# Performance work log

Measured on AMD Instinct MI355X. Metric: run time of the kernel, lower is better.

The kernel has to match this reference:

```python
import jax, jax.numpy as jnp
import numpy as np
import math

D = 768
H = 12
HD = D // H  # 64
B, N = 16, 1024
EPS = 1e-5


def _rope(x, cos, sin):
    # x: [B,N,H,hd]; cos,sin: [1,N,1,hd]
    x1, x2 = x[..., ::2], x[..., 1::2]
    return jnp.concatenate(
        [x1 * cos[..., ::2] - x2 * sin[..., ::2],
         x1 * sin[..., 1::2] + x2 * cos[..., 1::2]], axis=-1)


def setup_inputs() -> dict:
    key = jax.random.key(0)
    ks = jax.random.split(key, 8)
    s = 1.0 / math.sqrt(D)  # xavier-ish scale
    return {
        "x": jax.random.normal(ks[0], (B, N, D), jnp.float32),
        "rope_emb": jax.random.normal(ks[1], (N, HD), jnp.float32),
        "ln_w": jnp.ones((D,), jnp.float32),
        "ln_b": jnp.zeros((D,), jnp.float32),
        "enc_w": jax.random.normal(ks[2], (D, D), jnp.float32) * s,
        "enc_b": jnp.zeros((D,), jnp.float32),
        "qk_w": jax.random.normal(ks[3], (D, D), jnp.float32) * s,
        "qk_b": jnp.zeros((D,), jnp.float32),
        "v_w": jax.random.normal(ks[4], (D, D), jnp.float32) * s,
        "v_b": jnp.zeros((D,), jnp.float32),
        "out_w": jax.random.normal(ks[5], (D, D), jnp.float32) * s,
        "out_b": jnp.zeros((D,), jnp.float32),
        "gate_w": jax.random.normal(ks[6], (D, D), jnp.float32) * s,
        "gate_b": jnp.zeros((D,), jnp.float32),
    }


def reference(x, rope_emb, ln_w, ln_b, enc_w, enc_b, qk_w, qk_b,
              v_w, v_b, out_w, out_b, gate_w, gate_b):
    b, n, d = x.shape
    # Pre-LayerNorm
    mu = jnp.mean(x, axis=-1, keepdims=True)
    var = jnp.mean(jnp.square(x - mu), axis=-1, keepdims=True)
    x_norm = (x - mu) / jnp.sqrt(var + EPS) * ln_w + ln_b
    # sparse latent encoder
    x_latent = jax.nn.relu(x_norm @ enc_w.T + enc_b)
    qk = (x_latent @ qk_w.T + qk_b).reshape(b, n, H, HD)
    v = (x_latent @ v_w.T + v_b).reshape(b, n, H, HD)
    ang = rope_emb[:, :HD]
    cos = jnp.cos(ang)[None, :, None, :]
    sin = jnp.sin(ang)[None, :, None, :]
    qk = _rope(qk, cos, sin)
    # raw (softmax-free) attention, Q=K
    scores = jnp.einsum('bnhd,bmhd->bhnm', qk, qk) / math.sqrt(HD)
    attn = jnp.einsum('bhnm,bmhd->bnhd', scores, v).reshape(b, n, d)
    attn = attn @ out_w.T + out_b
    gate = jax.nn.sigmoid(x_norm @ gate_w.T + gate_b)
    return x + gate * attn
```

## Files before the change

### kernel.cpp

```cpp
#include <hip/hip_runtime.h>

typedef __bf16 bf16;
typedef __bf16 bf16x4 __attribute__((ext_vector_type(4)));
typedef __bf16 bf16x8 __attribute__((ext_vector_type(8)));
typedef float floatx4 __attribute__((ext_vector_type(4)));

#define DD 768
#define NH 12
#define HDIM 64
#define BB 16
#define NN 1024
#define MTOT (BB*NN)
#define WELEM (DD*DD)

__device__ __forceinline__ void async_cp16(const void* g, void* l) {
  __builtin_amdgcn_global_load_lds((const __attribute__((address_space(1))) void*)g,
                                   (__attribute__((address_space(3))) void*)l, 16, 0, 0);
}

__global__ __launch_bounds__(256) void ln_kernel(const float* __restrict__ x,
    const float* __restrict__ w, const float* __restrict__ b, bf16* __restrict__ A) {
  int row = blockIdx.x * 4 + (threadIdx.x >> 6);
  int lane = threadIdx.x & 63;
  const float4* xr = (const float4*)(x + (size_t)row * DD);
  float4 v[3];
  float s = 0.f;
#pragma unroll
  for (int i = 0; i < 3; i++) {
    v[i] = xr[lane + 64 * i];
    s += v[i].x + v[i].y + v[i].z + v[i].w;
  }
#pragma unroll
  for (int o = 32; o; o >>= 1) s += __shfl_xor(s, o);
  float mu = s * (1.f / 768.f);
  float vs = 0.f;
#pragma unroll
  for (int i = 0; i < 3; i++) {
    float dx;
    dx = v[i].x - mu; vs += dx * dx;
    dx = v[i].y - mu; vs += dx * dx;
    dx = v[i].z - mu; vs += dx * dx;
    dx = v[i].w - mu; vs += dx * dx;
  }
#pragma unroll
  for (int o = 32; o; o >>= 1) vs += __shfl_xor(vs, o);
  float rstd = rsqrtf(vs * (1.f / 768.f) + 1e-5f);
  const float4* wv = (const float4*)w;
  const float4* bv = (const float4*)b;
  bf16* Ar = A + (size_t)row * DD;
#pragma unroll
  for (int i = 0; i < 3; i++) {
    int c4 = lane + 64 * i;
    float4 ww = wv[c4], bb = bv[c4];
    bf16x4 pk;
    pk[0] = (bf16)((v[i].x - mu) * rstd * ww.x + bb.x);
    pk[1] = (bf16)((v[i].y - mu) * rstd * ww.y + bb.y);
    pk[2] = (bf16)((v[i].z - mu) * rstd * ww.z + bb.z);
    pk[3] = (bf16)((v[i].w - mu) * rstd * ww.w + bb.w);
    *(bf16x4*)(Ar + c4 * 4) = pk;
  }
}

__global__ __launch_bounds__(256) void convw_kernel(const float* __restrict__ w0,
    const float* __restrict__ w1, const float* __restrict__ w2,
    const float* __restrict__ w3, const float* __restrict__ w4, bf16* __restrict__ out) {
  int i = blockIdx.x * 256 + threadIdx.x;
  int which = i / (WELEM / 4);
  int off = (i % (WELEM / 4)) * 4;
  const float* s = which == 0 ? w0 : which == 1 ? w1 : which == 2 ? w2 : which == 3 ? w3 : w4;
  float4 v = *(const float4*)(s + off);
  bf16x4 pk;
  pk[0] = (bf16)v.x; pk[1] = (bf16)v.y; pk[2] = (bf16)v.z; pk[3] = (bf16)v.w;
  *(bf16x4*)(out + (size_t)i * 4) = pk;
}

template<int EPI>
__device__ __forceinline__ void gemm_body(
    int bm, int bn, int bnl,
    const bf16* __restrict__ Aop, const bf16* __restrict__ W,
    const float* __restrict__ bias,
    bf16* __restrict__ Cb, float* __restrict__ Cf,
    const float* __restrict__ Xres, const bf16* __restrict__ Gate,
    bf16* As, bf16* Bs) {
  int tid = threadIdx.x;
  int wave = tid >> 6, lane = tid & 63;
  int quad = lane >> 4, l16 = lane & 15;
  int wm = wave & 1, wn = wave >> 1;
  int srow = lane >> 2, scol = (lane & 3) * 8;

  const bf16* Ag = Aop + (size_t)(bm * 128 + srow) * DD + scol;
  const bf16* Bg = W + (size_t)(bn * 128 + srow) * DD + scol;

  floatx4 acc[4][4];
#pragma unroll
  for (int i = 0; i < 4; i++)
#pragma unroll
    for (int j = 0; j < 4; j++)
      acc[i][j] = (floatx4){0.f, 0.f, 0.f, 0.f};

  for (int k0 = 0; k0 < DD; k0 += 32) {
    __syncthreads();
#pragma unroll
    for (int it = 0; it < 2; it++) {
      int r0 = (it * 4 + wave) * 16;
      async_cp16(Ag + (size_t)r0 * DD + k0, &As[r0 * 32]);
      async_cp16(Bg + (size_t)r0 * DD + k0, &Bs[r0 * 32]);
    }
    __syncthreads();
    bf16x8 a[4], b[4];
#pragma unroll
    for (int i = 0; i < 4; i++) a[i] = *(const bf16x8*)&As[(wm * 64 + i * 16 + l16) * 32 + quad * 8];
#pragma unroll
    for (int i = 0; i < 4; i++) b[i] = *(const bf16x8*)&Bs[(wn * 64 + i * 16 + l16) * 32 + quad * 8];
    if (EPI == 2) {
#pragma unroll
      for (int mi = 0; mi < 4; mi++)
#pragma unroll
        for (int ni = 0; ni < 4; ni++)
          acc[mi][ni] = __builtin_amdgcn_mfma_f32_16x16x32_bf16(a[mi], b[ni], acc[mi][ni], 0, 0, 0);
    } else {
#pragma unroll
      for (int mi = 0; mi < 4; mi++)
#pragma unroll
        for (int ni = 0; ni < 4; ni++)
          acc[mi][ni] = __builtin_amdgcn_mfma_f32_16x16x32_bf16(b[ni], a[mi], acc[mi][ni], 0, 0, 0);
    }
  }

  if (EPI == 2) {
#pragma unroll
    for (int ni = 0; ni < 4; ni++) {
      int gc = bnl * 128 + wn * 64 + ni * 16 + l16;
      float bz = bias[gc];
      int h = gc >> 6, dd2 = gc & 63;
#pragma unroll
      for (int mi = 0; mi < 4; mi++) {
        int gm0 = bm * 128 + wm * 64 + mi * 16 + quad * 4;
        int b_ = gm0 >> 10, n0 = gm0 & 1023;
        bf16x4 pk;
#pragma unroll
        for (int r = 0; r < 4; r++) pk[r] = (bf16)(acc[mi][ni][r] + bz);
        *(bf16x4*)&Cb[(((size_t)b_ * NH + h) * HDIM + dd2) * NN + n0] = pk;
      }
    }
  } else {
#pragma unroll
    for (int mi = 0; mi < 4; mi++) {
      int gm = bm * 128 + wm * 64 + mi * 16 + l16;
#pragma unroll
      for (int ni = 0; ni < 4; ni++) {
        int gc = bnl * 128 + wn * 64 + ni * 16 + quad * 4;
        float4 bz = *(const float4*)&bias[gc];
        float v0 = acc[mi][ni][0] + bz.x;
        float v1 = acc[mi][ni][1] + bz.y;
        float v2 = acc[mi][ni][2] + bz.z;
        float v3 = acc[mi][ni][3] + bz.w;
        size_t idx = (size_t)gm * DD + gc;
        if (EPI == 4) {
          bf16x4 g = *(const bf16x4*)&Gate[idx];
          float4 xr = *(const float4*)&Xres[idx];
          float4 o;
          o.x = xr.x + (float)g[0] * v0;
          o.y = xr.y + (float)g[1] * v1;
          o.z = xr.z + (float)g[2] * v2;
          o.w = xr.w + (float)g[3] * v3;
          *(float4*)&Cf[idx] = o;
        } else {
          bf16x4 pk;
          if (EPI == 0) {
            pk[0] = (bf16)fmaxf(v0, 0.f); pk[1] = (bf16)fmaxf(v1, 0.f);
            pk[2] = (bf16)fmaxf(v2, 0.f); pk[3] = (bf16)fmaxf(v3, 0.f);
          } else if (EPI == 1) {
            pk[0] = (bf16)v0; pk[1] = (bf16)v1; pk[2] = (bf16)v2; pk[3] = (bf16)v3;
          } else {
            pk[0] = (bf16)(1.f / (1.f + __expf(-v0)));
            pk[1] = (bf16)(1.f / (1.f + __expf(-v1)));
            pk[2] = (bf16)(1.f / (1.f + __expf(-v2)));
            pk[3] = (bf16)(1.f / (1.f + __expf(-v3)));
          }
          *(bf16x4*)&Cb[idx] = pk;
        }
      }
    }
  }
}

template<int EPI_LO, int EPI_HI, int NBN>
__global__ __launch_bounds__(256) void gemm_kernel(
    const bf16* __restrict__ Aop, const bf16* __restrict__ W,
    const float* __restrict__ bias_lo, const float* __restrict__ bias_hi,
    bf16* __restrict__ C_lo, bf16* __restrict__ C_hi, float* __restrict__ Cf,
    const float* __restrict__ Xres, const bf16* __restrict__ Gate) {
  __shared__ bf16 As[128 * 32];
  __shared__ bf16 Bs[128 * 32];
  int blk = blockIdx.x;
  int xcd = blk & 7, slot = blk >> 3;
  int bm = xcd * 16 + slot / NBN;
  int bn = slot % NBN;
  if (NBN == 12 && bn >= 6) {
    gemm_body<EPI_HI>(bm, bn, bn - 6, Aop, W, bias_hi, C_hi, Cf, Xres, Gate, As, Bs);
  } else {
    gemm_body<EPI_LO>(bm, bn, bn, Aop, W, bias_lo, C_lo, Cf, Xres, Gate, As, Bs);
  }
}

__global__ __launch_bounds__(256) void rope_kernel(const bf16* __restrict__ QKraw,
    const float* __restrict__ rope, bf16* __restrict__ QKr, bf16* __restrict__ QKrT) {
  int blk = blockIdx.x;
  int bh = blk >> 7;
  int nc = blk & 127;
  int b_ = bh / NH, h_ = bh % NH;
  int t = threadIdx.x;
  int noff = t >> 5;
  int d = t & 31;
  int n = nc * 8 + noff;
  size_t ibase = ((size_t)(b_ * NN + n)) * DD + h_ * HDIM;
  float x1 = (float)QKraw[ibase + 2 * d];
  float x2 = (float)QKraw[ibase + 2 * d + 1];
  float a0 = rope[n * HDIM + 2 * d];
  float a1 = rope[n * HDIM + 2 * d + 1];
  float o1 = x1 * __cosf(a0) - x2 * __sinf(a0);
  float o2 = x1 * __sinf(a1) + x2 * __cosf(a1);
  size_t obase = ((size_t)(b_ * NN + n)) * DD + h_ * HDIM;
  QKr[obase + d] = (bf16)o1;
  QKr[obase + 32 + d] = (bf16)o2;
  size_t tbase = ((size_t)bh * HDIM + d) * NN + n;
  QKrT[tbase] = (bf16)o1;
  QKrT[tbase + (size_t)32 * NN] = (bf16)o2;
}

__global__ __launch_bounds__(256) void attn_kernel(const bf16* __restrict__ QKr,
    const bf16* __restrict__ QKrT, const bf16* __restrict__ VT, bf16* __restrict__ attn) {
  __shared__ float Tp[64][64];
  __shared__ bf16 Tbf[64][72];
  int bh = blockIdx.x;
  int tid = threadIdx.x, wave = tid >> 6, lane = tid & 63;
  int quad = lane >> 4, l16 = lane & 15;
  const bf16* Qt = QKrT + (size_t)bh * (HDIM * NN);
  const bf16* Vt = VT + (size_t)bh * (HDIM * NN);

  floatx4 acc[4][4];
#pragma unroll
  for (int i = 0; i < 4; i++)
#pragma unroll
    for (int j = 0; j < 4; j++)
      acc[i][j] = (floatx4){0.f, 0.f, 0.f, 0.f};

  int kbase = wave * 256;
#pragma unroll
  for (int k0 = 0; k0 < 256; k0 += 32) {
    bf16x8 a[4], b[4];
#pragma unroll
    for (int i = 0; i < 4; i++) a[i] = *(const bf16x8*)&Qt[(size_t)(i * 16 + l16) * NN + kbase + k0 + quad * 8];
#pragma unroll
    for (int i = 0; i < 4; i++) b[i] = *(const bf16x8*)&Vt[(size_t)(i * 16 + l16) * NN + kbase + k0 + quad * 8];
#pragma unroll
    for (int mi = 0; mi < 4; mi++)
#pragma unroll
      for (int ni = 0; ni < 4; ni++)
        acc[mi][ni] = __builtin_amdgcn_mfma_f32_16x16x32_bf16(a[mi], b[ni], acc[mi][ni], 0, 0, 0);
  }
#pragma unroll
  for (int w = 0; w < 4; w++) {
    if (wave == w) {
#pragma unroll
      for (int mi = 0; mi < 4; mi++)
#pragma unroll
        for (int ni = 0; ni < 4; ni++)
#pragma unroll
          for (int r = 0; r < 4; r++) {
            float val = acc[mi][ni][r];
            float* p = &Tp[mi * 16 + quad * 4 + r][ni * 16 + l16];
            if (w == 0) *p = val; else *p += val;
          }
    }
    __syncthreads();
  }
  for (int e = tid; e < 4096; e += 256) {
    int d1 = e >> 6, d2 = e & 63;
    Tbf[d2][d1] = (bf16)(Tp[d1][d2] * 0.125f);
  }
  __syncthreads();

  int b_ = bh / NH, h_ = bh % NH;
  const bf16* Q = QKr + (size_t)(b_ * NN) * DD + h_ * HDIM;
  bf16* Ao = attn + (size_t)(b_ * NN) * DD + h_ * HDIM;
  bf16x8 Bf[4][2];
#pragma unroll
  for (int ni = 0; ni < 4; ni++)
#pragma unroll
    for (int ks = 0; ks < 2; ks++)
      Bf[ni][ks] = *(const bf16x8*)&Tbf[ni * 16 + l16][ks * 32 + quad * 8];

  for (int mi = 0; mi < 16; mi++) {
    int nrow = wave * 256 + mi * 16;
    bf16x8 a0 = *(const bf16x8*)&Q[(size_t)(nrow + l16) * DD + quad * 8];
    bf16x8 a1 = *(const bf16x8*)&Q[(size_t)(nrow + l16) * DD + 32 + quad * 8];
    floatx4 o[4];
#pragma unroll
    for (int ni = 0; ni < 4; ni++) o[ni] = (floatx4){0.f, 0.f, 0.f, 0.f};
#pragma unroll
    for (int ni = 0; ni < 4; ni++) {
      o[ni] = __builtin_amdgcn_mfma_f32_16x16x32_bf16(a0, Bf[ni][0], o[ni], 0, 0, 0);
      o[ni] = __builtin_amdgcn_mfma_f32_16x16x32_bf16(a1, Bf[ni][1], o[ni], 0, 0, 0);
    }
#pragma unroll
    for (int ni = 0; ni < 4; ni++)
#pragma unroll
      for (int r = 0; r < 4; r++)
        Ao[(size_t)(nrow + quad * 4 + r) * DD + ni * 16 + l16] = (bf16)o[ni][r];
  }
}

extern "C" void kernel_launch(void* const* d_in, const int* in_sizes, int n_in,
                              void* d_out, int out_size, void* d_ws, size_t ws_size,
                              hipStream_t stream) {
  const float* x      = (const float*)d_in[0];
  const float* rope   = (const float*)d_in[1];
  const float* ln_w   = (const float*)d_in[2];
  const float* ln_b   = (const float*)d_in[3];
  const float* enc_w  = (const float*)d_in[4];
  const float* enc_b  = (const float*)d_in[5];
  const float* qk_w   = (const float*)d_in[6];
  const float* qk_b   = (const float*)d_in[7];
  const float* v_w    = (const float*)d_in[8];
  const float* v_b    = (const float*)d_in[9];
  const float* out_w  = (const float*)d_in[10];
  const float* out_b  = (const float*)d_in[11];
  const float* gate_w = (const float*)d_in[12];
  const float* gate_b = (const float*)d_in[13];

  char* w = (char*)d_ws;
  const size_t S = (size_t)MTOT * DD * 2;
  bf16* s0 = (bf16*)(w);
  bf16* s1 = (bf16*)(w + S);
  bf16* s2 = (bf16*)(w + 2 * S);
  bf16* s3 = (bf16*)(w + 3 * S);
  bf16* s4 = (bf16*)(w + 4 * S);
  bf16* s5 = (bf16*)(w + 5 * S);
  bf16* Wb = (bf16*)(w + 6 * S);

  bf16* A = s0;
  bf16* L = s1;
  bf16* Gate = s2;
  bf16* QKraw = s0;
  bf16* QKr = s3;
  bf16* QKrT = s4;
  bf16* VT = s5;
  bf16* attnb = s1;

  ln_kernel<<<dim3(MTOT / 4), dim3(256), 0, stream>>>(x, ln_w, ln_b, A);
  convw_kernel<<<dim3(5 * WELEM / 4 / 256), dim3(256), 0, stream>>>(enc_w, gate_w, qk_w, v_w, out_w, Wb);

  gemm_kernel<0, 3, 12><<<dim3(1536), dim3(256), 0, stream>>>(
      A, Wb, enc_b, gate_b, L, Gate, nullptr, nullptr, nullptr);
  gemm_kernel<1, 2, 12><<<dim3(1536), dim3(256), 0, stream>>>(
      L, Wb + 2 * (size_t)WELEM, qk_b, v_b, QKraw, VT, nullptr, nullptr, nullptr);
  rope_kernel<<<dim3(BB * NH * 128), dim3(256), 0, stream>>>(QKraw, rope, QKr, QKrT);
  attn_kernel<<<dim3(BB * NH), dim3(256), 0, stream>>>(QKr, QKrT, VT, attnb);
  gemm_kernel<4, 4, 6><<<dim3(768), dim3(256), 0, stream>>>(
      attnb, Wb + 4 * (size_t)WELEM, out_b, nullptr, nullptr, nullptr, (float*)d_out, x, Gate);
}
```

Measured before the change: 360.0 us.

## Widen GEMM K-tile with swizzled LDS, vectorize rope transpose, split attention blocks

The GEMM main loop now stages 64-wide K tiles with an XOR-swizzled LDS layout, which halves the barrier count and avoids bank conflicts on fragment reads. The rope kernel processes 128 rows per block with vectorized loads and sincos, and writes the transposed copy through LDS so the global stores are coalesced. The attention kernel launches four blocks per head with XCD-aware mapping, spreading the output phase across more CUs, but each block recomputes the 64x64 K^T V product. LDS use per GEMM block doubles, which may lower occupancy.

```diff
diff --git a/kernel.cpp b/kernel.cpp
--- a/kernel.cpp
+++ b/kernel.cpp
@@ -86,10 +86,11 @@
   int wave = tid >> 6, lane = tid & 63;
   int quad = lane >> 4, l16 = lane & 15;
   int wm = wave & 1, wn = wave >> 1;
-  int srow = lane >> 2, scol = (lane & 3) * 8;
-
-  const bf16* Ag = Aop + (size_t)(bm * 128 + srow) * DD + scol;
-  const bf16* Bg = W + (size_t)(bn * 128 + srow) * DD + scol;
+  int sr = lane >> 3;
+  int smcg = (lane & 7) ^ sr;
+
+  const bf16* Ag = Aop + (size_t)(bm * 128) * DD;
+  const bf16* Bg = W + (size_t)(bn * 128) * DD;
 
   floatx4 acc[4][4];
 #pragma unroll
@@ -98,32 +99,39 @@
     for (int j = 0; j < 4; j++)
       acc[i][j] = (floatx4){0.f, 0.f, 0.f, 0.f};
 
-  for (int k0 = 0; k0 < DD; k0 += 32) {
+  int swzA = (l16 & 7);
+
+  for (int k0 = 0; k0 < DD; k0 += 64) {
     __syncthreads();
 #pragma unroll
-    for (int it = 0; it < 2; it++) {
-      int r0 = (it * 4 + wave) * 16;
-      async_cp16(Ag + (size_t)r0 * DD + k0, &As[r0 * 32]);
-      async_cp16(Bg + (size_t)r0 * DD + k0, &Bs[r0 * 32]);
+    for (int it = 0; it < 4; it++) {
+      int c = it * 4 + wave;
+      int row = c * 8 + sr;
+      async_cp16(Ag + (size_t)row * DD + k0 + smcg * 8, &As[c * 512]);
+      async_cp16(Bg + (size_t)row * DD + k0 + smcg * 8, &Bs[c * 512]);
     }
     __syncthreads();
-    bf16x8 a[4], b[4];
-#pragma unroll
-    for (int i = 0; i < 4; i++) a[i] = *(const bf16x8*)&As[(wm * 64 + i * 16 + l16) * 32 + quad * 8];
-#pragma unroll
-    for (int i = 0; i < 4; i++) b[i] = *(const bf16x8*)&Bs[(wn * 64 + i * 16 + l16) * 32 + quad * 8];
-    if (EPI == 2) {
-#pragma unroll
-      for (int mi = 0; mi < 4; mi++)
-#pragma unroll
-        for (int ni = 0; ni < 4; ni++)
-          acc[mi][ni] = __builtin_amdgcn_mfma_f32_16x16x32_bf16(a[mi], b[ni], acc[mi][ni], 0, 0, 0);
-    } else {
-#pragma unroll
-      for (int mi = 0; mi < 4; mi++)
-#pragma unroll
-        for (int ni = 0; ni < 4; ni++)
-          acc[mi][ni] = __builtin_amdgcn_mfma_f32_16x16x32_bf16(b[ni], a[mi], acc[mi][ni], 0, 0, 0);
+#pragma unroll
+    for (int ks = 0; ks < 2; ks++) {
+      int cg = (ks * 4 + quad) ^ swzA;
+      bf16x8 a[4], b[4];
+#pragma unroll
+      for (int i = 0; i < 4; i++) a[i] = *(const bf16x8*)&As[(wm * 64 + i * 16 + l16) * 64 + cg * 8];
+#pragma unroll
+      for (int i = 0; i < 4; i++) b[i] = *(const bf16x8*)&Bs[(wn * 64 + i * 16 + l16) * 64 + cg * 8];
+      if (EPI == 2) {
+#pragma unroll
+        for (int mi = 0; mi < 4; mi++)
+#pragma unroll
+          for (int ni = 0; ni < 4; ni++)
+            acc[mi][ni] = __builtin_amdgcn_mfma_f32_16x16x32_bf16(a[mi], b[ni], acc[mi][ni], 0, 0, 0);
+      } else {
+#pragma unroll
+        for (int mi = 0; mi < 4; mi++)
+#pragma unroll
+          for (int ni = 0; ni < 4; ni++)
+            acc[mi][ni] = __builtin_amdgcn_mfma_f32_16x16x32_bf16(b[ni], a[mi], acc[mi][ni], 0, 0, 0);
+      }
     }
   }
 
@@ -191,8 +199,8 @@
     const float* __restrict__ bias_lo, const float* __restrict__ bias_hi,
     bf16* __restrict__ C_lo, bf16* __restrict__ C_hi, float* __restrict__ Cf,
     const float* __restrict__ Xres, const bf16* __restrict__ Gate) {
-  __shared__ bf16 As[128 * 32];
-  __shared__ bf16 Bs[128 * 32];
+  __shared__ bf16 As[128 * 64];
+  __shared__ bf16 Bs[128 * 64];
   int blk = blockIdx.x;
   int xcd = blk & 7, slot = blk >> 3;
   int bm = xcd * 16 + slot / NBN;
@@ -204,36 +212,73 @@
   }
 }
 
+#define TLS_S 132
 __global__ __launch_bounds__(256) void rope_kernel(const bf16* __restrict__ QKraw,
     const float* __restrict__ rope, bf16* __restrict__ QKr, bf16* __restrict__ QKrT) {
+  __shared__ bf16 Tls[64 * TLS_S];
   int blk = blockIdx.x;
-  int bh = blk >> 7;
-  int nc = blk & 127;
+  int bh = blk >> 3, nc = blk & 7;
   int b_ = bh / NH, h_ = bh % NH;
+  int nbase = nc * 128;
   int t = threadIdx.x;
-  int noff = t >> 5;
-  int d = t & 31;
-  int n = nc * 8 + noff;
-  size_t ibase = ((size_t)(b_ * NN + n)) * DD + h_ * HDIM;
-  float x1 = (float)QKraw[ibase + 2 * d];
-  float x2 = (float)QKraw[ibase + 2 * d + 1];
-  float a0 = rope[n * HDIM + 2 * d];
-  float a1 = rope[n * HDIM + 2 * d + 1];
-  float o1 = x1 * __cosf(a0) - x2 * __sinf(a0);
-  float o2 = x1 * __sinf(a1) + x2 * __cosf(a1);
-  size_t obase = ((size_t)(b_ * NN + n)) * DD + h_ * HDIM;
-  QKr[obase + d] = (bf16)o1;
-  QKr[obase + 32 + d] = (bf16)o2;
-  size_t tbase = ((size_t)bh * HDIM + d) * NN + n;
-  QKrT[tbase] = (bf16)o1;
-  QKrT[tbase + (size_t)32 * NN] = (bf16)o2;
+  {
+    int n_loc = t >> 1, ch = t & 1;
+    int n = nbase + n_loc;
+    const bf16* src = QKraw + ((size_t)(b_ * NN + n)) * DD + h_ * HDIM + ch * 32;
+    const float* rp = rope + n * HDIM + ch * 32;
+    __attribute__((aligned(16))) bf16 o1[16];
+    __attribute__((aligned(16))) bf16 o2[16];
+#pragma unroll
+    for (int i0 = 0; i0 < 4; i0++) {
+      bf16x8 v = *(const bf16x8*)(src + i0 * 8);
+      float4 r0 = *(const float4*)(rp + i0 * 8);
+      float4 r1 = *(const float4*)(rp + i0 * 8 + 4);
+      float a0s[4] = {r0.x, r0.z, r1.x, r1.z};
+      float a1s[4] = {r0.y, r0.w, r1.y, r1.w};
+#pragma unroll
+      for (int p = 0; p < 4; p++) {
+        float x1 = (float)v[2 * p], x2 = (float)v[2 * p + 1];
+        float s0, c0, s1, c1;
+        __sincosf(a0s[p], &s0, &c0);
+        __sincosf(a1s[p], &s1, &c1);
+        int d = i0 * 4 + p;
+        o1[d] = (bf16)(x1 * c0 - x2 * s0);
+        o2[d] = (bf16)(x1 * s1 + x2 * c1);
+      }
+    }
+    bf16* dst = QKr + ((size_t)(b_ * NN + n)) * DD + h_ * HDIM;
+    *(bf16x8*)&dst[ch * 16]      = *(bf16x8*)&o1[0];
+    *(bf16x8*)&dst[ch * 16 + 8]  = *(bf16x8*)&o1[8];
+    *(bf16x8*)&dst[32 + ch * 16]     = *(bf16x8*)&o2[0];
+    *(bf16x8*)&dst[32 + ch * 16 + 8] = *(bf16x8*)&o2[8];
+#pragma unroll
+    for (int d = 0; d < 16; d++) {
+      Tls[(ch * 16 + d) * TLS_S + n_loc] = o1[d];
+      Tls[(32 + ch * 16 + d) * TLS_S + n_loc] = o2[d];
+    }
+  }
+  __syncthreads();
+  {
+    int c = t >> 2, qn = t & 3;
+    __attribute__((aligned(16))) bf16 buf[32];
+#pragma unroll
+    for (int j = 0; j < 8; j++)
+      *(bf16x4*)&buf[j * 4] = *(const bf16x4*)&Tls[c * TLS_S + qn * 32 + j * 4];
+    bf16* dst = QKrT + ((size_t)bh * HDIM + c) * NN + nbase + qn * 32;
+#pragma unroll
+    for (int j = 0; j < 4; j++)
+      *(bf16x8*)&dst[j * 8] = *(bf16x8*)&buf[j * 8];
+  }
 }
 
 __global__ __launch_bounds__(256) void attn_kernel(const bf16* __restrict__ QKr,
     const bf16* __restrict__ QKrT, const bf16* __restrict__ VT, bf16* __restrict__ attn) {
   __shared__ float Tp[64][64];
   __shared__ bf16 Tbf[64][72];
-  int bh = blockIdx.x;
+  int blk = blockIdx.x;
+  int xcd = blk & 7, s = blk >> 3;
+  int bhl = s >> 2, q = s & 3;
+  int bh = xcd * 24 + bhl;
   int tid = threadIdx.x, wave = tid >> 6, lane = tid & 63;
   int quad = lane >> 4, l16 = lane & 15;
   const bf16* Qt = QKrT + (size_t)bh * (HDIM * NN);
@@ -292,8 +337,9 @@
     for (int ks = 0; ks < 2; ks++)
       Bf[ni][ks] = *(const bf16x8*)&Tbf[ni * 16 + l16][ks * 32 + quad * 8];
 
-  for (int mi = 0; mi < 16; mi++) {
-    int nrow = wave * 256 + mi * 16;
+#pragma unroll
+  for (int mi = 0; mi < 4; mi++) {
+    int nrow = q * 256 + wave * 64 + mi * 16;
     bf16x8 a0 = *(const bf16x8*)&Q[(size_t)(nrow + l16) * DD + quad * 8];
     bf16x8 a1 = *(const bf16x8*)&Q[(size_t)(nrow + l16) * DD + 32 + quad * 8];
     floatx4 o[4];
@@ -356,8 +402,8 @@
       A, Wb, enc_b, gate_b, L, Gate, nullptr, nullptr, nullptr);
   gemm_kernel<1, 2, 12><<<dim3(1536), dim3(256), 0, stream>>>(
       L, Wb + 2 * (size_t)WELEM, qk_b, v_b, QKraw, VT, nullptr, nullptr, nullptr);
-  rope_kernel<<<dim3(BB * NH * 128), dim3(256), 0, stream>>>(QKraw, rope, QKr, QKrT);
-  attn_kernel<<<dim3(BB * NH), dim3(256), 0, stream>>>(QKr, QKrT, VT, attnb);
+  rope_kernel<<<dim3(BB * NH * 8), dim3(256), 0, stream>>>(QKraw, rope, QKr, QKrT);
+  attn_kernel<<<dim3(BB * NH * 4), dim3(256), 0, stream>>>(QKr, QKrT, VT, attnb);
   gemm_kernel<4, 4, 6><<<dim3(768), dim3(256), 0, stream>>>(
       attnb, Wb + 4 * (size_t)WELEM, out_b, nullptr, nullptr, nullptr, (float*)d_out, x, Gate);
 }
```

Result: faster. 339.8 us (-5.6%).

## Fuse prep kernels and RoPE epilogue, double-buffer GEMM, split attention across blocks

Applied to the files above, without the earlier changes.

Merges layernorm and weight conversion into one launch, and folds RoPE into the QK GEMM epilogue, which removes the separate rope kernel and the transposed QK/V buffers. The GEMM gains double-buffered LDS staging with an XOR swizzle and a launch-bounds occupancy hint. Attention now transposes Q and V through LDS inside the kernel and splits each head across 4 blocks (768 instead of 192), so more CUs are busy. The cost is that each of the 4 blocks recomputes the 64x64 K^T V product redundantly, and LDS use is higher.

```diff
diff --git a/kernel.cpp b/kernel.cpp
--- a/kernel.cpp
+++ b/kernel.cpp
@@ -1,6 +1,7 @@
 #include <hip/hip_runtime.h>
 
 typedef __bf16 bf16;
+typedef __bf16 bf16x2 __attribute__((ext_vector_type(2)));
 typedef __bf16 bf16x4 __attribute__((ext_vector_type(4)));
 typedef __bf16 bf16x8 __attribute__((ext_vector_type(8)));
 typedef float floatx4 __attribute__((ext_vector_type(4)));
@@ -18,67 +19,69 @@
                                    (__attribute__((address_space(3))) void*)l, 16, 0, 0);
 }
 
-__global__ __launch_bounds__(256) void ln_kernel(const float* __restrict__ x,
-    const float* __restrict__ w, const float* __restrict__ b, bf16* __restrict__ A) {
-  int row = blockIdx.x * 4 + (threadIdx.x >> 6);
-  int lane = threadIdx.x & 63;
-  const float4* xr = (const float4*)(x + (size_t)row * DD);
-  float4 v[3];
-  float s = 0.f;
-#pragma unroll
-  for (int i = 0; i < 3; i++) {
-    v[i] = xr[lane + 64 * i];
-    s += v[i].x + v[i].y + v[i].z + v[i].w;
-  }
-#pragma unroll
-  for (int o = 32; o; o >>= 1) s += __shfl_xor(s, o);
-  float mu = s * (1.f / 768.f);
-  float vs = 0.f;
-#pragma unroll
-  for (int i = 0; i < 3; i++) {
-    float dx;
-    dx = v[i].x - mu; vs += dx * dx;
-    dx = v[i].y - mu; vs += dx * dx;
-    dx = v[i].z - mu; vs += dx * dx;
-    dx = v[i].w - mu; vs += dx * dx;
-  }
-#pragma unroll
-  for (int o = 32; o; o >>= 1) vs += __shfl_xor(vs, o);
-  float rstd = rsqrtf(vs * (1.f / 768.f) + 1e-5f);
-  const float4* wv = (const float4*)w;
-  const float4* bv = (const float4*)b;
-  bf16* Ar = A + (size_t)row * DD;
-#pragma unroll
-  for (int i = 0; i < 3; i++) {
-    int c4 = lane + 64 * i;
-    float4 ww = wv[c4], bb = bv[c4];
+__global__ __launch_bounds__(256) void prep_kernel(const float* __restrict__ x,
+    const float* __restrict__ lnw, const float* __restrict__ lnb, bf16* __restrict__ A,
+    const float* __restrict__ w0, const float* __restrict__ w1, const float* __restrict__ w2,
+    const float* __restrict__ w3, const float* __restrict__ w4, bf16* __restrict__ Wb) {
+  int blk = blockIdx.x;
+  if (blk < 4096) {
+    int row = blk * 4 + (threadIdx.x >> 6);
+    int lane = threadIdx.x & 63;
+    const float4* xr = (const float4*)(x + (size_t)row * DD);
+    float4 v[3];
+    float s = 0.f;
+#pragma unroll
+    for (int i = 0; i < 3; i++) {
+      v[i] = xr[lane + 64 * i];
+      s += v[i].x + v[i].y + v[i].z + v[i].w;
+    }
+#pragma unroll
+    for (int o = 32; o; o >>= 1) s += __shfl_xor(s, o);
+    float mu = s * (1.f / 768.f);
+    float vs = 0.f;
+#pragma unroll
+    for (int i = 0; i < 3; i++) {
+      float dx;
+      dx = v[i].x - mu; vs += dx * dx;
+      dx = v[i].y - mu; vs += dx * dx;
+      dx = v[i].z - mu; vs += dx * dx;
+      dx = v[i].w - mu; vs += dx * dx;
+    }
+#pragma unroll
+    for (int o = 32; o; o >>= 1) vs += __shfl_xor(vs, o);
+    float rstd = rsqrtf(vs * (1.f / 768.f) + 1e-5f);
+    const float4* wv = (const float4*)lnw;
+    const float4* bv = (const float4*)lnb;
+    bf16* Ar = A + (size_t)row * DD;
+#pragma unroll
+    for (int i = 0; i < 3; i++) {
+      int c4 = lane + 64 * i;
+      float4 ww = wv[c4], bb = bv[c4];
+      bf16x4 pk;
+      pk[0] = (bf16)((v[i].x - mu) * rstd * ww.x + bb.x);
+      pk[1] = (bf16)((v[i].y - mu) * rstd * ww.y + bb.y);
+      pk[2] = (bf16)((v[i].z - mu) * rstd * ww.z + bb.z);
+      pk[3] = (bf16)((v[i].w - mu) * rstd * ww.w + bb.w);
+      *(bf16x4*)(Ar + c4 * 4) = pk;
+    }
+  } else {
+    int i = (blk - 4096) * 256 + threadIdx.x;
+    int which = i / (WELEM / 4);
+    int off = (i % (WELEM / 4)) * 4;
+    const float* s = which == 0 ? w0 : which == 1 ? w1 : which == 2 ? w2 : which == 3 ? w3 : w4;
+    float4 v = *(const float4*)(s + off);
     bf16x4 pk;
-    pk[0] = (bf16)((v[i].x - mu) * rstd * ww.x + bb.x);
-    pk[1] = (bf16)((v[i].y - mu) * rstd * ww.y + bb.y);
-    pk[2] = (bf16)((v[i].z - mu) * rstd * ww.z + bb.z);
-    pk[3] = (bf16)((v[i].w - mu) * rstd * ww.w + bb.w);
-    *(bf16x4*)(Ar + c4 * 4) = pk;
-  }
-}
-
-__global__ __launch_bounds__(256) void convw_kernel(const float* __restrict__ w0,
-    const float* __restrict__ w1, const float* __restrict__ w2,
-    const float* __restrict__ w3, const float* __restrict__ w4, bf16* __restrict__ out) {
-  int i = blockIdx.x * 256 + threadIdx.x;
-  int which = i / (WELEM / 4);
-  int off = (i % (WELEM / 4)) * 4;
-  const float* s = which == 0 ? w0 : which == 1 ? w1 : which == 2 ? w2 : which == 3 ? w3 : w4;
-  float4 v = *(const float4*)(s + off);
-  bf16x4 pk;
-  pk[0] = (bf16)v.x; pk[1] = (bf16)v.y; pk[2] = (bf16)v.z; pk[3] = (bf16)v.w;
-  *(bf16x4*)(out + (size_t)i * 4) = pk;
-}
-
+    pk[0] = (bf16)v.x; pk[1] = (bf16)v.y; pk[2] = (bf16)v.z; pk[3] = (bf16)v.w;
+    *(bf16x4*)(Wb + (size_t)i * 4) = pk;
+  }
+}
+
+#define STG32 4096
 template<int EPI>
 __device__ __forceinline__ void gemm_body(
     int bm, int bn, int bnl,
     const bf16* __restrict__ Aop, const bf16* __restrict__ W,
-    const float* __restrict__ bias,
+    const float* __restrict__ bias, const float* __restrict__ rope,
     bf16* __restrict__ Cb, float* __restrict__ Cf,
     const float* __restrict__ Xres, const bf16* __restrict__ Gate,
     bf16* As, bf16* Bs) {
@@ -86,10 +89,11 @@
   int wave = tid >> 6, lane = tid & 63;
   int quad = lane >> 4, l16 = lane & 15;
   int wm = wave & 1, wn = wave >> 1;
-  int srow = lane >> 2, scol = (lane & 3) * 8;
-
-  const bf16* Ag = Aop + (size_t)(bm * 128 + srow) * DD + scol;
-  const bf16* Bg = W + (size_t)(bn * 128 + srow) * DD + scol;
+  int srow = lane >> 2;
+  int scg = (lane & 3) ^ ((lane >> 3) & 3);
+
+  const bf16* Ag = Aop + ((size_t)(bm * 128) + srow) * DD + scg * 8;
+  const bf16* Bg = W + ((size_t)(bn * 128) + srow) * DD + scg * 8;
 
   floatx4 acc[4][4];
 #pragma unroll
@@ -98,204 +102,197 @@
     for (int j = 0; j < 4; j++)
       acc[i][j] = (floatx4){0.f, 0.f, 0.f, 0.f};
 
-  for (int k0 = 0; k0 < DD; k0 += 32) {
+  int swz = (l16 >> 1) & 3;
+
+#pragma unroll
+  for (int it = 0; it < 2; it++) {
+    int c = it * 4 + wave;
+    async_cp16(Ag + (size_t)(c * 16) * DD, &As[c * 512]);
+    async_cp16(Bg + (size_t)(c * 16) * DD, &Bs[c * 512]);
+  }
+
+  for (int i = 0; i < 24; i++) {
     __syncthreads();
-#pragma unroll
-    for (int it = 0; it < 2; it++) {
-      int r0 = (it * 4 + wave) * 16;
-      async_cp16(Ag + (size_t)r0 * DD + k0, &As[r0 * 32]);
-      async_cp16(Bg + (size_t)r0 * DD + k0, &Bs[r0 * 32]);
-    }
-    __syncthreads();
+    if (i < 23) {
+      int k0 = (i + 1) * 32;
+      int so = ((i + 1) & 1) * STG32;
+#pragma unroll
+      for (int it = 0; it < 2; it++) {
+        int c = it * 4 + wave;
+        async_cp16(Ag + (size_t)(c * 16) * DD + k0, &As[so + c * 512]);
+        async_cp16(Bg + (size_t)(c * 16) * DD + k0, &Bs[so + c * 512]);
+      }
+    }
+    int bo = (i & 1) * STG32;
+    int cg = quad ^ swz;
     bf16x8 a[4], b[4];
 #pragma unroll
-    for (int i = 0; i < 4; i++) a[i] = *(const bf16x8*)&As[(wm * 64 + i * 16 + l16) * 32 + quad * 8];
-#pragma unroll
-    for (int i = 0; i < 4; i++) b[i] = *(const bf16x8*)&Bs[(wn * 64 + i * 16 + l16) * 32 + quad * 8];
-    if (EPI == 2) {
-#pragma unroll
-      for (int mi = 0; mi < 4; mi++)
-#pragma unroll
-        for (int ni = 0; ni < 4; ni++)
-          acc[mi][ni] = __builtin_amdgcn_mfma_f32_16x16x32_bf16(a[mi], b[ni], acc[mi][ni], 0, 0, 0);
-    } else {
-#pragma unroll
-      for (int mi = 0; mi < 4; mi++)
-#pragma unroll
-        for (int ni = 0; ni < 4; ni++)
-          acc[mi][ni] = __builtin_amdgcn_mfma_f32_16x16x32_bf16(b[ni], a[mi], acc[mi][ni], 0, 0, 0);
-    }
-  }
-
-  if (EPI == 2) {
+    for (int j = 0; j < 4; j++) a[j] = *(const bf16x8*)&As[bo + (wm * 64 + j * 16 + l16) * 32 + cg * 8];
+#pragma unroll
+    for (int j = 0; j < 4; j++) b[j] = *(const bf16x8*)&Bs[bo + (wn * 64 + j * 16 + l16) * 32 + cg * 8];
+#pragma unroll
+    for (int mi = 0; mi < 4; mi++)
+#pragma unroll
+      for (int ni = 0; ni < 4; ni++)
+        acc[mi][ni] = __builtin_amdgcn_mfma_f32_16x16x32_bf16(b[ni], a[mi], acc[mi][ni], 0, 0, 0);
+  }
+
+#pragma unroll
+  for (int mi = 0; mi < 4; mi++) {
+    int gm = bm * 128 + wm * 64 + mi * 16 + l16;
 #pragma unroll
     for (int ni = 0; ni < 4; ni++) {
-      int gc = bnl * 128 + wn * 64 + ni * 16 + l16;
-      float bz = bias[gc];
-      int h = gc >> 6, dd2 = gc & 63;
-#pragma unroll
-      for (int mi = 0; mi < 4; mi++) {
-        int gm0 = bm * 128 + wm * 64 + mi * 16 + quad * 4;
-        int b_ = gm0 >> 10, n0 = gm0 & 1023;
+      int gc = bnl * 128 + wn * 64 + ni * 16 + quad * 4;
+      float4 bz = *(const float4*)&bias[gc];
+      float v0 = acc[mi][ni][0] + bz.x;
+      float v1 = acc[mi][ni][1] + bz.y;
+      float v2 = acc[mi][ni][2] + bz.z;
+      float v3 = acc[mi][ni][3] + bz.w;
+      size_t idx = (size_t)gm * DD + gc;
+      if (EPI == 4) {
+        bf16x4 g = *(const bf16x4*)&Gate[idx];
+        float4 xr = *(const float4*)&Xres[idx];
+        float4 o;
+        o.x = xr.x + (float)g[0] * v0;
+        o.y = xr.y + (float)g[1] * v1;
+        o.z = xr.z + (float)g[2] * v2;
+        o.w = xr.w + (float)g[3] * v3;
+        *(float4*)&Cf[idx] = o;
+      } else if (EPI == 5) {
+        int n = gm & (NN - 1);
+        int h = gc >> 6, c0 = gc & 63;
+        int j0 = c0 >> 1;
+        float4 ang = *(const float4*)&rope[n * HDIM + c0];
+        float s0, cc0, s1, cc1, s2, cc2, s3, cc3;
+        __sincosf(ang.x, &s0, &cc0);
+        __sincosf(ang.y, &s1, &cc1);
+        __sincosf(ang.z, &s2, &cc2);
+        __sincosf(ang.w, &s3, &cc3);
+        bf16x2 lo, hi;
+        lo[0] = (bf16)(v0 * cc0 - v1 * s0);
+        lo[1] = (bf16)(v2 * cc2 - v3 * s2);
+        hi[0] = (bf16)(v0 * s1 + v1 * cc1);
+        hi[1] = (bf16)(v2 * s3 + v3 * cc3);
+        bf16* base = Cb + (size_t)gm * DD + h * HDIM;
+        *(bf16x2*)&base[j0] = lo;
+        *(bf16x2*)&base[32 + j0] = hi;
+      } else {
         bf16x4 pk;
-#pragma unroll
-        for (int r = 0; r < 4; r++) pk[r] = (bf16)(acc[mi][ni][r] + bz);
-        *(bf16x4*)&Cb[(((size_t)b_ * NH + h) * HDIM + dd2) * NN + n0] = pk;
+        if (EPI == 0) {
+          pk[0] = (bf16)fmaxf(v0, 0.f); pk[1] = (bf16)fmaxf(v1, 0.f);
+          pk[2] = (bf16)fmaxf(v2, 0.f); pk[3] = (bf16)fmaxf(v3, 0.f);
+        } else if (EPI == 1) {
+          pk[0] = (bf16)v0; pk[1] = (bf16)v1; pk[2] = (bf16)v2; pk[3] = (bf16)v3;
+        } else {
+          pk[0] = (bf16)(1.f / (1.f + __expf(-v0)));
+          pk[1] = (bf16)(1.f / (1.f + __expf(-v1)));
+          pk[2] = (bf16)(1.f / (1.f + __expf(-v2)));
+          pk[3] = (bf16)(1.f / (1.f + __expf(-v3)));
+        }
+        *(bf16x4*)&Cb[idx] = pk;
       }
     }
-  } else {
-#pragma unroll
-    for (int mi = 0; mi < 4; mi++) {
-      int gm = bm * 128 + wm * 64 + mi * 16 + l16;
-#pragma unroll
-      for (int ni = 0; ni < 4; ni++) {
-        int gc = bnl * 128 + wn * 64 + ni * 16 + quad * 4;
-        float4 bz = *(const float4*)&bias[gc];
-        float v0 = acc[mi][ni][0] + bz.x;
-        float v1 = acc[mi][ni][1] + bz.y;
-        float v2 = acc[mi][ni][2] + bz.z;
-        float v3 = acc[mi][ni][3] + bz.w;
-        size_t idx = (size_t)gm * DD + gc;
-        if (EPI == 4) {
-          bf16x4 g = *(const bf16x4*)&Gate[idx];
-          float4 xr = *(const float4*)&Xres[idx];
-          float4 o;
-          o.x = xr.x + (float)g[0] * v0;
-          o.y = xr.y + (float)g[1] * v1;
-          o.z = xr.z + (float)g[2] * v2;
-          o.w = xr.w + (float)g[3] * v3;
-          *(float4*)&Cf[idx] = o;
-        } else {
-          bf16x4 pk;
-          if (EPI == 0) {
-            pk[0] = (bf16)fmaxf(v0, 0.f); pk[1] = (bf16)fmaxf(v1, 0.f);
-            pk[2] = (bf16)fmaxf(v2, 0.f); pk[3] = (bf16)fmaxf(v3, 0.f);
-          } else if (EPI == 1) {
-            pk[0] = (bf16)v0; pk[1] = (bf16)v1; pk[2] = (bf16)v2; pk[3] = (bf16)v3;
-          } else {
-            pk[0] = (bf16)(1.f / (1.f + __expf(-v0)));
-            pk[1] = (bf16)(1.f / (1.f + __expf(-v1)));
-            pk[2] = (bf16)(1.f / (1.f + __expf(-v2)));
-            pk[3] = (bf16)(1.f / (1.f + __expf(-v3)));
-          }
-          *(bf16x4*)&Cb[idx] = pk;
-        }
-      }
-    }
   }
 }
 
 template<int EPI_LO, int EPI_HI, int NBN>
-__global__ __launch_bounds__(256) void gemm_kernel(
+__global__ __launch_bounds__(256, 4) void gemm_kernel(
     const bf16* __restrict__ Aop, const bf16* __restrict__ W,
     const float* __restrict__ bias_lo, const float* __restrict__ bias_hi,
+    const float* __restrict__ rope,
     bf16* __restrict__ C_lo, bf16* __restrict__ C_hi, float* __restrict__ Cf,
     const float* __restrict__ Xres, const bf16* __restrict__ Gate) {
-  __shared__ bf16 As[128 * 32];
-  __shared__ bf16 Bs[128 * 32];
+  __shared__ bf16 As[2 * STG32];
+  __shared__ bf16 Bs[2 * STG32];
   int blk = blockIdx.x;
   int xcd = blk & 7, slot = blk >> 3;
   int bm = xcd * 16 + slot / NBN;
   int bn = slot % NBN;
   if (NBN == 12 && bn >= 6) {
-    gemm_body<EPI_HI>(bm, bn, bn - 6, Aop, W, bias_hi, C_hi, Cf, Xres, Gate, As, Bs);
+    gemm_body<EPI_HI>(bm, bn, bn - 6, Aop, W, bias_hi, rope, C_hi, Cf, Xres, Gate, As, Bs);
   } else {
-    gemm_body<EPI_LO>(bm, bn, bn, Aop, W, bias_lo, C_lo, Cf, Xres, Gate, As, Bs);
-  }
-}
-
-__global__ __launch_bounds__(256) void rope_kernel(const bf16* __restrict__ QKraw,
-    const float* __restrict__ rope, bf16* __restrict__ QKr, bf16* __restrict__ QKrT) {
+    gemm_body<EPI_LO>(bm, bn, bn, Aop, W, bias_lo, rope, C_lo, Cf, Xres, Gate, As, Bs);
+  }
+}
+
+#define TQS 136
+__global__ __launch_bounds__(256, 2) void attn_kernel(const bf16* __restrict__ QKr,
+    const bf16* __restrict__ V, bf16* __restrict__ attn) {
+  __shared__ bf16 Qt[64 * TQS];
+  __shared__ bf16 Vt[64 * TQS];
+  __shared__ bf16 Tbf[64 * 72];
   int blk = blockIdx.x;
-  int bh = blk >> 7;
-  int nc = blk & 127;
+  int xcd = blk & 7, s = blk >> 3;
+  int bhl = s >> 2, q = s & 3;
+  int bh = xcd * 24 + bhl;
   int b_ = bh / NH, h_ = bh % NH;
-  int t = threadIdx.x;
-  int noff = t >> 5;
-  int d = t & 31;
-  int n = nc * 8 + noff;
-  size_t ibase = ((size_t)(b_ * NN + n)) * DD + h_ * HDIM;
-  float x1 = (float)QKraw[ibase + 2 * d];
-  float x2 = (float)QKraw[ibase + 2 * d + 1];
-  float a0 = rope[n * HDIM + 2 * d];
-  float a1 = rope[n * HDIM + 2 * d + 1];
-  float o1 = x1 * __cosf(a0) - x2 * __sinf(a0);
-  float o2 = x1 * __sinf(a1) + x2 * __cosf(a1);
-  size_t obase = ((size_t)(b_ * NN + n)) * DD + h_ * HDIM;
-  QKr[obase + d] = (bf16)o1;
-  QKr[obase + 32 + d] = (bf16)o2;
-  size_t tbase = ((size_t)bh * HDIM + d) * NN + n;
-  QKrT[tbase] = (bf16)o1;
-  QKrT[tbase + (size_t)32 * NN] = (bf16)o2;
-}
-
-__global__ __launch_bounds__(256) void attn_kernel(const bf16* __restrict__ QKr,
-    const bf16* __restrict__ QKrT, const bf16* __restrict__ VT, bf16* __restrict__ attn) {
-  __shared__ float Tp[64][64];
-  __shared__ bf16 Tbf[64][72];
-  int bh = blockIdx.x;
   int tid = threadIdx.x, wave = tid >> 6, lane = tid & 63;
   int quad = lane >> 4, l16 = lane & 15;
-  const bf16* Qt = QKrT + (size_t)bh * (HDIM * NN);
-  const bf16* Vt = VT + (size_t)bh * (HDIM * NN);
-
-  floatx4 acc[4][4];
-#pragma unroll
-  for (int i = 0; i < 4; i++)
-#pragma unroll
-    for (int j = 0; j < 4; j++)
-      acc[i][j] = (floatx4){0.f, 0.f, 0.f, 0.f};
-
-  int kbase = wave * 256;
-#pragma unroll
-  for (int k0 = 0; k0 < 256; k0 += 32) {
-    bf16x8 a[4], b[4];
-#pragma unroll
-    for (int i = 0; i < 4; i++) a[i] = *(const bf16x8*)&Qt[(size_t)(i * 16 + l16) * NN + kbase + k0 + quad * 8];
-#pragma unroll
-    for (int i = 0; i < 4; i++) b[i] = *(const bf16x8*)&Vt[(size_t)(i * 16 + l16) * NN + kbase + k0 + quad * 8];
-#pragma unroll
-    for (int mi = 0; mi < 4; mi++)
-#pragma unroll
-      for (int ni = 0; ni < 4; ni++)
-        acc[mi][ni] = __builtin_amdgcn_mfma_f32_16x16x32_bf16(a[mi], b[ni], acc[mi][ni], 0, 0, 0);
-  }
-#pragma unroll
-  for (int w = 0; w < 4; w++) {
-    if (wave == w) {
-#pragma unroll
-      for (int mi = 0; mi < 4; mi++)
-#pragma unroll
-        for (int ni = 0; ni < 4; ni++)
-#pragma unroll
-          for (int r = 0; r < 4; r++) {
-            float val = acc[mi][ni][r];
-            float* p = &Tp[mi * 16 + quad * 4 + r][ni * 16 + l16];
-            if (w == 0) *p = val; else *p += val;
-          }
-    }
+
+  const bf16* Qbase = QKr + (size_t)(b_ * NN) * DD + h_ * HDIM;
+  const bf16* Vbase = V + (size_t)(b_ * NN) * DD + h_ * HDIM;
+
+  floatx4 acc1[4];
+#pragma unroll
+  for (int i = 0; i < 4; i++) acc1[i] = (floatx4){0.f, 0.f, 0.f, 0.f};
+
+  int p = tid & 63, dq = tid >> 6;
+
+  for (int c = 0; c < 8; c++) {
+    int n0 = c * 128 + p * 2;
+    bf16x8 q0a = *(const bf16x8*)&Qbase[(size_t)n0 * DD + dq * 16];
+    bf16x8 q0b = *(const bf16x8*)&Qbase[(size_t)n0 * DD + dq * 16 + 8];
+    bf16x8 q1a = *(const bf16x8*)&Qbase[(size_t)(n0 + 1) * DD + dq * 16];
+    bf16x8 q1b = *(const bf16x8*)&Qbase[(size_t)(n0 + 1) * DD + dq * 16 + 8];
+    bf16x8 v0a = *(const bf16x8*)&Vbase[(size_t)n0 * DD + dq * 16];
+    bf16x8 v0b = *(const bf16x8*)&Vbase[(size_t)n0 * DD + dq * 16 + 8];
+    bf16x8 v1a = *(const bf16x8*)&Vbase[(size_t)(n0 + 1) * DD + dq * 16];
+    bf16x8 v1b = *(const bf16x8*)&Vbase[(size_t)(n0 + 1) * DD + dq * 16 + 8];
     __syncthreads();
-  }
-  for (int e = tid; e < 4096; e += 256) {
-    int d1 = e >> 6, d2 = e & 63;
-    Tbf[d2][d1] = (bf16)(Tp[d1][d2] * 0.125f);
+    int nl = p * 2;
+#pragma unroll
+    for (int j = 0; j < 8; j++) {
+      bf16x2 qa; qa[0] = q0a[j]; qa[1] = q1a[j];
+      bf16x2 qb; qb[0] = q0b[j]; qb[1] = q1b[j];
+      bf16x2 va; va[0] = v0a[j]; va[1] = v1a[j];
+      bf16x2 vb; vb[0] = v0b[j]; vb[1] = v1b[j];
+      *(bf16x2*)&Qt[(dq * 16 + j) * TQS + nl] = qa;
+      *(bf16x2*)&Qt[(dq * 16 + 8 + j) * TQS + nl] = qb;
+      *(bf16x2*)&Vt[(dq * 16 + j) * TQS + nl] = va;
+      *(bf16x2*)&Vt[(dq * 16 + 8 + j) * TQS + nl] = vb;
+    }
+    __syncthreads();
+#pragma unroll
+    for (int ks = 0; ks < 4; ks++) {
+      bf16x8 a = *(const bf16x8*)&Qt[(wave * 16 + l16) * TQS + ks * 32 + quad * 8];
+#pragma unroll
+      for (int ni = 0; ni < 4; ni++) {
+        bf16x8 b = *(const bf16x8*)&Vt[(ni * 16 + l16) * TQS + ks * 32 + quad * 8];
+        acc1[ni] = __builtin_amdgcn_mfma_f32_16x16x32_bf16(a, b, acc1[ni], 0, 0, 0);
+      }
+    }
   }
   __syncthreads();
-
-  int b_ = bh / NH, h_ = bh % NH;
-  const bf16* Q = QKr + (size_t)(b_ * NN) * DD + h_ * HDIM;
+#pragma unroll
+  for (int ni = 0; ni < 4; ni++)
+#pragma unroll
+    for (int r = 0; r < 4; r++)
+      Tbf[(ni * 16 + l16) * 72 + wave * 16 + quad * 4 + r] = (bf16)(acc1[ni][r] * 0.125f);
+  __syncthreads();
+
   bf16* Ao = attn + (size_t)(b_ * NN) * DD + h_ * HDIM;
   bf16x8 Bf[4][2];
 #pragma unroll
   for (int ni = 0; ni < 4; ni++)
 #pragma unroll
     for (int ks = 0; ks < 2; ks++)
-      Bf[ni][ks] = *(const bf16x8*)&Tbf[ni * 16 + l16][ks * 32 + quad * 8];
-
-  for (int mi = 0; mi < 16; mi++) {
-    int nrow = wave * 256 + mi * 16;
-    bf16x8 a0 = *(const bf16x8*)&Q[(size_t)(nrow + l16) * DD + quad * 8];
-    bf16x8 a1 = *(const bf16x8*)&Q[(size_t)(nrow + l16) * DD + 32 + quad * 8];
+      Bf[ni][ks] = *(const bf16x8*)&Tbf[(ni * 16 + l16) * 72 + ks * 32 + quad * 8];
+
+#pragma unroll
+  for (int mi = 0; mi < 4; mi++) {
+    int nrow = q * 256 + wave * 64 + mi * 16;
+    bf16x8 a0 = *(const bf16x8*)&Qbase[(size_t)(nrow + l16) * DD + quad * 8];
+    bf16x8 a1 = *(const bf16x8*)&Qbase[(size_t)(nrow + l16) * DD + 32 + quad * 8];
     floatx4 o[4];
 #pragma unroll
     for (int ni = 0; ni < 4; ni++) o[ni] = (floatx4){0.f, 0.f, 0.f, 0.f};
@@ -332,32 +329,23 @@
 
   char* w = (char*)d_ws;
   const size_t S = (size_t)MTOT * DD * 2;
-  bf16* s0 = (bf16*)(w);
-  bf16* s1 = (bf16*)(w + S);
-  bf16* s2 = (bf16*)(w + 2 * S);
-  bf16* s3 = (bf16*)(w + 3 * S);
-  bf16* s4 = (bf16*)(w + 4 * S);
-  bf16* s5 = (bf16*)(w + 5 * S);
-  bf16* Wb = (bf16*)(w + 6 * S);
-
-  bf16* A = s0;
-  bf16* L = s1;
-  bf16* Gate = s2;
-  bf16* QKraw = s0;
-  bf16* QKr = s3;
-  bf16* QKrT = s4;
-  bf16* VT = s5;
-  bf16* attnb = s1;
-
-  ln_kernel<<<dim3(MTOT / 4), dim3(256), 0, stream>>>(x, ln_w, ln_b, A);
-  convw_kernel<<<dim3(5 * WELEM / 4 / 256), dim3(256), 0, stream>>>(enc_w, gate_w, qk_w, v_w, out_w, Wb);
+  bf16* A     = (bf16*)(w);
+  bf16* L     = (bf16*)(w + S);
+  bf16* Gate  = (bf16*)(w + 2 * S);
+  bf16* QKr   = (bf16*)(w + 3 * S);
+  bf16* Vb    = (bf16*)(w + 4 * S);
+  bf16* Wb    = (bf16*)(w + 6 * S);
+  bf16* attnb = L;
+
+  prep_kernel<<<dim3(4096 + 2880), dim3(256), 0, stream>>>(
+      x, ln_w, ln_b, A, enc_w, gate_w, qk_w, v_w, out_w, Wb);
 
   gemm_kernel<0, 3, 12><<<dim3(1536), dim3(256), 0, stream>>>(
-      A, Wb, enc_b, gate_b, L, Gate, nullptr, nullptr, nullptr);
-  gemm_kernel<1, 2, 12><<<dim3(1536), dim3(256), 0, stream>>>(
-      L, Wb + 2 * (size_t)WELEM, qk_b, v_b, QKraw, VT, nullptr, nullptr, nullptr);
-  rope_kernel<<<dim3(BB * NH * 128), dim3(256), 0, stream>>>(QKraw, rope, QKr, QKrT);
-  attn_kernel<<<dim3(BB * NH), dim3(256), 0, stream>>>(QKr, QKrT, VT, attnb);
+      A, Wb, enc_b, gate_b, nullptr, L, Gate, nullptr, nullptr, nullptr);
+  gemm_kernel<5, 1, 12><<<dim3(1536), dim3(256), 0, stream>>>(
+      L, Wb + 2 * (size_t)WELEM, qk_b, v_b, rope, QKr, Vb, nullptr, nullptr, nullptr);
+  attn_kernel<<<dim3(768), dim3(256), 0, stream>>>(QKr, Vb, attnb);
   gemm_kernel<4, 4, 6><<<dim3(768), dim3(256), 0, stream>>>(
-      attnb, Wb + 4 * (size_t)WELEM, out_b, nullptr, nullptr, nullptr, (float*)d_out, x, Gate);
-}
+      attnb, Wb + 4 * (size_t)WELEM, out_b, nullptr, nullptr, nullptr, nullptr,
+      (float*)d_out, x, Gate);
+}
```

New measurement: 344.4 us. -4.3%, faster.
